# Kernel tuning notes

Hardware: AMD Instinct MI355X
Metric: run time of the kernel (lower is better)

## Reference

```python
import jax, jax.numpy as jnp
import numpy as np

B = 256      # batch
G = 16       # groups
GS = 588     # hard-coded group_size
HID = 1024   # hidden_dim (forced = hidden_dim3)
FEAT = 2048  # hidden_dim4 = per-group output feature dim


def setup_inputs() -> dict:
    key = jax.random.key(0)
    ks = jax.random.split(key, 16)
    def w(k, shape, fan_in):
        return jax.random.normal(k, shape, jnp.float32) / np.float32(np.sqrt(fan_in))
    inp = {
        "q": jax.random.normal(ks[0], (B, G * GS), jnp.float32),
        "k": jax.random.normal(ks[1], (B, G * GS), jnp.float32),
        # stacked per-group q-branch SVF weights: fc1 [G,GS,HID], fc4 [G,HID,FEAT]
        "Wq1": w(ks[2], (G, GS, HID), GS),
        "bq1": jnp.zeros((G, HID), jnp.float32),
        "Wq4": w(ks[3], (G, HID, FEAT), HID),
        "bq4": jnp.zeros((G, FEAT), jnp.float32),
        # stacked per-group k-branch SVF weights
        "Wk1": w(ks[4], (G, GS, HID), GS),
        "bk1": jnp.zeros((G, HID), jnp.float32),
        "Wk4": w(ks[5], (G, HID, FEAT), HID),
        "bk4": jnp.zeros((G, FEAT), jnp.float32),
        # shared global SVF: fc1 [G*FEAT, HID], fc4 [HID, FEAT]
        "Wg1": w(ks[6], (G * FEAT, HID), G * FEAT),
        "bg1": jnp.zeros((HID,), jnp.float32),
        "Wg4": w(ks[7], (HID, FEAT), HID),
        "bg4": jnp.zeros((FEAT,), jnp.float32),
    }
    return inp


def _grouped_svf(x, W1, b1, W4, b4):
    # x: [B, G*GS] -> per-group contiguous slices, batched grouped GEMMs
    xg = x.reshape(B, G, GS)
    h = jax.nn.silu(jnp.einsum('bgd,gdh->bgh', xg, W1) + b1)   # [B,G,HID]
    f = jax.nn.silu(jnp.einsum('bgh,gho->bgo', h, W4) + b4)    # [B,G,FEAT]
    # torch.stack(dim=2).view(B,-1): feature-major interleave [B, FEAT, G] -> flat
    return jnp.transpose(f, (0, 2, 1)).reshape(B, FEAT * G)


def _global_svf(x, Wg1, bg1, Wg4, bg4):
    h = jax.nn.silu(x @ Wg1 + bg1)      # [B, HID]
    return jax.nn.silu(h @ Wg4 + bg4)   # [B, FEAT]


def reference(q, k, Wq1, bq1, Wq4, bq4, Wk1, bk1, Wk4, bk4, Wg1, bg1, Wg4, bg4):
    qf = _grouped_svf(q, Wq1, bq1, Wq4, bq4)
    kf = _grouped_svf(k, Wk1, bk1, Wk4, bk4)
    q_out = _global_svf(qf, Wg1, bg1, Wg4, bg4)
    k_out = _global_svf(kf, Wg1, bg1, Wg4, bg4)
    scores = jnp.sum(q_out * k_out, axis=-1)   # [B]
    # faithful to original: softmax over the batch dimension
    return jax.nn.softmax(scores, axis=-1)
```

## Files before the change

### kernel.cpp

```cpp
#include <hip/hip_runtime.h>


#define CB 256
#define CG 16
#define CGS 588
#define CHID 1024
#define CFEAT 2048

typedef __attribute__((ext_vector_type(8))) short bf16x8;
typedef __attribute__((ext_vector_type(4))) float f32x4;

__device__ __forceinline__ int lds_addr(int row, int kcol) {
  return row * 64 + ((((kcol >> 3) ^ ((row >> 1) & 3)) << 4) | ((kcol & 7) << 1));
}

__device__ __forceinline__ void split4(const float4& v, uint2& hi, uint2& lo) {
  unsigned u0 = __float_as_uint(v.x), u1 = __float_as_uint(v.y);
  unsigned u2 = __float_as_uint(v.z), u3 = __float_as_uint(v.w);
  unsigned h0 = u0 & 0xffff0000u, h1 = u1 & 0xffff0000u;
  unsigned h2 = u2 & 0xffff0000u, h3 = u3 & 0xffff0000u;
  hi.x = (h0 >> 16) | h1;
  hi.y = (h2 >> 16) | h3;
  float r0 = v.x - __uint_as_float(h0), r1 = v.y - __uint_as_float(h1);
  float r2 = v.z - __uint_as_float(h2), r3 = v.w - __uint_as_float(h3);
  lo.x = (__float_as_uint(r0) >> 16) | (__float_as_uint(r1) & 0xffff0000u);
  lo.y = (__float_as_uint(r2) >> 16) | (__float_as_uint(r3) & 0xffff0000u);
}

__device__ __forceinline__ float silu_f(float x) {
  return x / (1.f + __expf(-x));
}

template <int GROUPED, int PERMUTE, int EPILOGUE>
__global__ __launch_bounds__(256, 2) void gemm_k(
    const float* __restrict__ A0, const float* __restrict__ A1,
    const float* __restrict__ B0, const float* __restrict__ B1,
    const float* __restrict__ bias0, const float* __restrict__ bias1,
    float* __restrict__ C, int K, int lda, int ldb, int ldc, int a_goff,
    long a_broff, long b_gstride, int bias_gstride, long c_broff, int c_goff,
    long c_sstride, int nksteps) {
  __shared__ __align__(16) char sm[32768];
  constexpr int A_HI = 0, A_LO = 8192, B_HI = 16384, B_LO = 24576;
  const int tid = threadIdx.x;
  const int m0 = blockIdx.x * 128, n0 = blockIdx.y * 128;

  const float* Ap;
  const float* Bp;
  const float* bp = nullptr;
  float* Cb;
  int acol = 0;
  int kbase = 0;
  if (GROUPED) {
    int z = blockIdx.z;
    int br = z >> 4, g = z & 15;
    Ap = (br ? A1 : A0) + (long)br * a_broff;
    Bp = (br ? B1 : B0) + (long)g * b_gstride;
    if (EPILOGUE) bp = (br ? bias1 : bias0) + (long)g * bias_gstride;
    Cb = C + (long)br * c_broff + (long)g * c_goff;
    acol = g * a_goff;
  } else {
    Ap = A0;
    Bp = B0;
    bp = bias0;
    Cb = C + (long)blockIdx.z * c_sstride;
    kbase = (int)blockIdx.z * nksteps * 32;
  }

  float4 ga[4];
  float gb[4][4];

  auto tload = [&](int k0) {
    const int r = tid >> 3, c4 = (tid & 7) << 2;
    const int gk = k0 + c4;
    #pragma unroll
    for (int i = 0; i < 4; ++i) {
      if (gk < K)
        ga[i] = *reinterpret_cast<const float4*>(Ap + (long)(m0 + i * 32 + r) * lda + acol + gk);
      else
        ga[i] = make_float4(0.f, 0.f, 0.f, 0.f);
    }
    const int n = tid & 127, kq0 = (tid >> 7) << 2;
    #pragma unroll
    for (int i = 0; i < 4; ++i) {
      #pragma unroll
      for (int j = 0; j < 4; ++j) {
        int kk = k0 + i * 8 + kq0 + j;
        float v = 0.f;
        if (kk < K) {
          long brow = PERMUTE ? (long)(((kk & 2047) << 4) | (kk >> 11)) : (long)kk;
          v = Bp[brow * ldb + n0 + n];
        }
        gb[i][j] = v;
      }
    }
  };

  auto tstore = [&]() {
    const int r = tid >> 3, c4 = (tid & 7) << 2;
    #pragma unroll
    for (int i = 0; i < 4; ++i) {
      uint2 h, l;
      split4(ga[i], h, l);
      int ad = lds_addr(i * 32 + r, c4);
      *reinterpret_cast<uint2*>(sm + A_HI + ad) = h;
      *reinterpret_cast<uint2*>(sm + A_LO + ad) = l;
    }
    const int n = tid & 127, kq0 = (tid >> 7) << 2;
    #pragma unroll
    for (int i = 0; i < 4; ++i) {
      float4 v = make_float4(gb[i][0], gb[i][1], gb[i][2], gb[i][3]);
      uint2 h, l;
      split4(v, h, l);
      int ad = lds_addr(n, i * 8 + kq0);
      *reinterpret_cast<uint2*>(sm + B_HI + ad) = h;
      *reinterpret_cast<uint2*>(sm + B_LO + ad) = l;
    }
  };

  f32x4 acc[4][4];
  #pragma unroll
  for (int a = 0; a < 4; ++a)
    #pragma unroll
    for (int b = 0; b < 4; ++b) acc[a][b] = (f32x4){0.f, 0.f, 0.f, 0.f};

  const int lane = tid & 63, w = tid >> 6;
  const int wr = w >> 1, wc = w & 1;
  const int fr = lane & 15, kb = lane >> 4;

  tload(kbase);
  for (int s = 0; s < nksteps; ++s) {
    tstore();
    __syncthreads();
    if (s + 1 < nksteps) tload(kbase + (s + 1) * 32);

    bf16x8 ah[4], al[4], bh[4], bl[4];
    #pragma unroll
    for (int f = 0; f < 4; ++f) {
      int row = wr * 64 + f * 16 + fr;
      int ad = row * 64 + ((kb ^ ((row >> 1) & 3)) << 4);
      ah[f] = *reinterpret_cast<const bf16x8*>(sm + A_HI + ad);
      al[f] = *reinterpret_cast<const bf16x8*>(sm + A_LO + ad);
      int rob = wc * 64 + f * 16 + fr;
      int bd = rob * 64 + ((kb ^ ((rob >> 1) & 3)) << 4);
      bh[f] = *reinterpret_cast<const bf16x8*>(sm + B_HI + bd);
      bl[f] = *reinterpret_cast<const bf16x8*>(sm + B_LO + bd);
    }
    #pragma unroll
    for (int im = 0; im < 4; ++im) {
      #pragma unroll
      for (int jn = 0; jn < 4; ++jn) {
        acc[im][jn] = __builtin_amdgcn_mfma_f32_16x16x32_bf16(ah[im], bh[jn], acc[im][jn], 0, 0, 0);
        acc[im][jn] = __builtin_amdgcn_mfma_f32_16x16x32_bf16(ah[im], bl[jn], acc[im][jn], 0, 0, 0);
        acc[im][jn] = __builtin_amdgcn_mfma_f32_16x16x32_bf16(al[im], bh[jn], acc[im][jn], 0, 0, 0);
      }
    }
    __syncthreads();
  }

  #pragma unroll
  for (int jn = 0; jn < 4; ++jn) {
    int col = n0 + wc * 64 + jn * 16 + fr;
    float bv = EPILOGUE ? bp[col] : 0.f;
    #pragma unroll
    for (int im = 0; im < 4; ++im) {
      int row0 = m0 + wr * 64 + im * 16 + kb * 4;
      #pragma unroll
      for (int j = 0; j < 4; ++j) {
        float x = acc[im][jn][j];
        if (EPILOGUE)
          Cb[(long)(row0 + j) * ldc + col] = silu_f(x + bv);
        else
          Cb[(long)(row0 + j) * ldc + col] = x;
      }
    }
  }
}

__global__ __launch_bounds__(256) void reduce_silu_k(
    const float* __restrict__ part, const float* __restrict__ bias,
    float* __restrict__ out, long MN, int N, int S) {
  long idx = ((long)blockIdx.x * blockDim.x + threadIdx.x) * 4;
  long stride = (long)gridDim.x * blockDim.x * 4;
  for (; idx < MN; idx += stride) {
    float4 a = make_float4(0.f, 0.f, 0.f, 0.f);
    for (int s = 0; s < S; ++s) {
      float4 p = *reinterpret_cast<const float4*>(&part[(long)s * MN + idx]);
      a.x += p.x; a.y += p.y; a.z += p.z; a.w += p.w;
    }
    int col = (int)(idx & (N - 1));
    float4 b = *reinterpret_cast<const float4*>(&bias[col]);
    float4 o;
    o.x = silu_f(a.x + b.x);
    o.y = silu_f(a.y + b.y);
    o.z = silu_f(a.z + b.z);
    o.w = silu_f(a.w + b.w);
    *reinterpret_cast<float4*>(&out[idx]) = o;
  }
}

__global__ __launch_bounds__(256) void scores_k(const float* __restrict__ out2,
                                                float* __restrict__ scores) {
  int b = blockIdx.x;
  const float* qo = out2 + (long)b * CFEAT;
  const float* ko = out2 + (long)(b + CB) * CFEAT;
  float s = 0.f;
  for (int i = threadIdx.x * 4; i < CFEAT; i += 1024) {
    float4 a = *reinterpret_cast<const float4*>(&qo[i]);
    float4 c = *reinterpret_cast<const float4*>(&ko[i]);
    s += a.x * c.x + a.y * c.y + a.z * c.z + a.w * c.w;
  }
  #pragma unroll
  for (int o = 32; o; o >>= 1) s += __shfl_down(s, o, 64);
  __shared__ float red[4];
  if ((threadIdx.x & 63) == 0) red[threadIdx.x >> 6] = s;
  __syncthreads();
  if (threadIdx.x == 0) scores[b] = red[0] + red[1] + red[2] + red[3];
}

__global__ __launch_bounds__(256) void softmax_k(const float* __restrict__ scores,
                                                 float* __restrict__ out) {
  int t = threadIdx.x;
  float v = scores[t];
  float m = v;
  #pragma unroll
  for (int o = 32; o; o >>= 1) m = fmaxf(m, __shfl_xor(m, o, 64));
  __shared__ float redm[4];
  if ((t & 63) == 0) redm[t >> 6] = m;
  __syncthreads();
  m = fmaxf(fmaxf(redm[0], redm[1]), fmaxf(redm[2], redm[3]));
  float e = __expf(v - m);
  float s = e;
  #pragma unroll
  for (int o = 32; o; o >>= 1) s += __shfl_xor(s, o, 64);
  __shared__ float reds[4];
  if ((t & 63) == 0) reds[t >> 6] = s;
  __syncthreads();
  s = reds[0] + reds[1] + reds[2] + reds[3];
  out[t] = e / s;
}

extern "C" void kernel_launch(void* const* d_in, const int* in_sizes, int n_in,
                              void* d_out, int out_size, void* d_ws,
                              size_t ws_size, hipStream_t stream) {
  const float* q   = (const float*)d_in[0];
  const float* kx  = (const float*)d_in[1];
  const float* Wq1 = (const float*)d_in[2];
  const float* bq1 = (const float*)d_in[3];
  const float* Wq4 = (const float*)d_in[4];
  const float* bq4 = (const float*)d_in[5];
  const float* Wk1 = (const float*)d_in[6];
  const float* bk1 = (const float*)d_in[7];
  const float* Wk4 = (const float*)d_in[8];
  const float* bk4 = (const float*)d_in[9];
  const float* Wg1 = (const float*)d_in[10];
  const float* bg1 = (const float*)d_in[11];
  const float* Wg4 = (const float*)d_in[12];
  const float* bg4 = (const float*)d_in[13];
  float* out = (float*)d_out;
  char* ws = (char*)d_ws;

  float* hqk   = (float*)(ws);
  float* fqk   = (float*)(ws + 33554432);
  float* part3 = (float*)(ws);
  float* h2    = (float*)(ws + 16777216);
  float* scors = (float*)(ws + 18874368);
  float* part4 = (float*)(ws + 33554432);
  float* out2  = (float*)(ws + 50331648);

  dim3 blk(256);

  gemm_k<1, 0, 1><<<dim3(2, 8, 32), blk, 0, stream>>>(
      q, kx, Wq1, Wk1, bq1, bk1, hqk,  CGS,  CG * CGS,
       CHID,  CG * CHID,  CGS,  0L,
       (long)CGS * CHID,  CHID,
       (long)CB * CG * CHID,  CHID, 0L,  19);

  gemm_k<1, 0, 1><<<dim3(2, 16, 32), blk, 0, stream>>>(
      hqk, hqk, Wq4, Wk4, bq4, bk4, fqk,  CHID,  CG * CHID,
       CFEAT,  CG * CFEAT,  CHID,
       (long)CB * CG * CHID,  (long)CHID * CFEAT,
       CFEAT,  (long)CB * CG * CFEAT,  CFEAT, 0L,
       32);

  gemm_k<0, 1, 0><<<dim3(4, 8, 8), blk, 0, stream>>>(
      fqk, fqk, Wg1, Wg1, bg1, bg1, part3,  CG * CFEAT,  CG * CFEAT,
       CHID,  CHID, 0, 0L, 0L, 0, 0L, 0,
       (long)512 * CHID,  128);
  reduce_silu_k<<<512, blk, 0, stream>>>(part3, bg1, h2, (long)512 * CHID, CHID, 8);

  gemm_k<0, 0, 0><<<dim3(4, 16, 4), blk, 0, stream>>>(
      h2, h2, Wg4, Wg4, bg4, bg4, part4,  CHID,  CHID,
       CFEAT,  CFEAT, 0, 0L, 0L, 0, 0L, 0,
       (long)512 * CFEAT,  8);
  reduce_silu_k<<<1024, blk, 0, stream>>>(part4, bg4, out2, (long)512 * CFEAT, CFEAT, 4);

  scores_k<<<256, blk, 0, stream>>>(out2, scors);
  softmax_k<<<1, blk, 0, stream>>>(scors, out);
}
```

Baseline: 753.9 us.

## Store intermediates as pre-split bf16 hi/lo planes and double split-K

Producer epilogues and the reduce kernel now write activations as separate bf16 high and low planes instead of fp32. Consumer GEMMs load these planes directly into LDS, which skips the per-tile split work and moves the same number of bytes per element. The split-K factor for both global GEMMs is also doubled, giving more blocks but more partial-sum traffic for the reduce kernels. Epilogue stores are scalar 2-byte writes to two planes, which may coalesce poorly.

New measurement: 1.043 ms. 1.38x slower.

```diff
diff --git a/kernel.cpp b/kernel.cpp
--- a/kernel.cpp
+++ b/kernel.cpp
@@ -31,12 +31,12 @@
   return x / (1.f + __expf(-x));
 }
 
-template <int GROUPED, int PERMUTE, int EPILOGUE>
+template <int GROUPED, int PERMUTE, int ASPLIT, int EPI>
 __global__ __launch_bounds__(256, 2) void gemm_k(
-    const float* __restrict__ A0, const float* __restrict__ A1,
+    const void* A0v, const void* A1v, long a_plane,
     const float* __restrict__ B0, const float* __restrict__ B1,
     const float* __restrict__ bias0, const float* __restrict__ bias1,
-    float* __restrict__ C, int K, int lda, int ldb, int ldc, int a_goff,
+    void* Cv, long c_plane, int K, int lda, int ldb, int ldc, int a_goff,
     long a_broff, long b_gstride, int bias_gstride, long c_broff, int c_goff,
     long c_sstride, int nksteps) {
   __shared__ __align__(16) char sm[32768];
@@ -44,40 +44,58 @@
   const int tid = threadIdx.x;
   const int m0 = blockIdx.x * 128, n0 = blockIdx.y * 128;
 
-  const float* Ap;
   const float* Bp;
   const float* bp = nullptr;
-  float* Cb;
+  const float* Af = nullptr;
+  const short* Ah = nullptr;
+  float* Cf = nullptr;
+  short* Chi = nullptr;
   int acol = 0;
   int kbase = 0;
   if (GROUPED) {
     int z = blockIdx.z;
     int br = z >> 4, g = z & 15;
-    Ap = (br ? A1 : A0) + (long)br * a_broff;
+    if (ASPLIT) Ah = (const short*)(br ? A1v : A0v) + (long)br * a_broff;
+    else        Af = (const float*)(br ? A1v : A0v) + (long)br * a_broff;
     Bp = (br ? B1 : B0) + (long)g * b_gstride;
-    if (EPILOGUE) bp = (br ? bias1 : bias0) + (long)g * bias_gstride;
-    Cb = C + (long)br * c_broff + (long)g * c_goff;
+    if (EPI) bp = (br ? bias1 : bias0) + (long)g * bias_gstride;
+    long coff = (long)br * c_broff + (long)g * c_goff;
+    if (EPI == 2) Chi = (short*)Cv + coff;
+    else          Cf = (float*)Cv + coff;
     acol = g * a_goff;
   } else {
-    Ap = A0;
+    if (ASPLIT) Ah = (const short*)A0v;
+    else        Af = (const float*)A0v;
     Bp = B0;
     bp = bias0;
-    Cb = C + (long)blockIdx.z * c_sstride;
+    if (EPI == 2) Chi = (short*)Cv;
+    else          Cf = (float*)Cv + (long)blockIdx.z * c_sstride;
     kbase = (int)blockIdx.z * nksteps * 32;
   }
 
   float4 ga[4];
+  uint4 gah[2], gal[2];
   float gb[4][4];
 
   auto tload = [&](int k0) {
-    const int r = tid >> 3, c4 = (tid & 7) << 2;
-    const int gk = k0 + c4;
-    #pragma unroll
-    for (int i = 0; i < 4; ++i) {
-      if (gk < K)
-        ga[i] = *reinterpret_cast<const float4*>(Ap + (long)(m0 + i * 32 + r) * lda + acol + gk);
-      else
-        ga[i] = make_float4(0.f, 0.f, 0.f, 0.f);
+    if (ASPLIT) {
+      #pragma unroll
+      for (int i = 0; i < 2; ++i) {
+        int u = tid + 256 * i, row = u >> 2, kq = u & 3;
+        long eo = (long)(m0 + row) * lda + acol + k0 + kq * 8;
+        gah[i] = *reinterpret_cast<const uint4*>(Ah + eo);
+        gal[i] = *reinterpret_cast<const uint4*>(Ah + a_plane + eo);
+      }
+    } else {
+      const int r = tid >> 3, c4 = (tid & 7) << 2;
+      const int gk = k0 + c4;
+      #pragma unroll
+      for (int i = 0; i < 4; ++i) {
+        if (gk < K)
+          ga[i] = *reinterpret_cast<const float4*>(Af + (long)(m0 + i * 32 + r) * lda + acol + gk);
+        else
+          ga[i] = make_float4(0.f, 0.f, 0.f, 0.f);
+      }
     }
     const int n = tid & 127, kq0 = (tid >> 7) << 2;
     #pragma unroll
@@ -96,14 +114,24 @@
   };
 
   auto tstore = [&]() {
-    const int r = tid >> 3, c4 = (tid & 7) << 2;
-    #pragma unroll
-    for (int i = 0; i < 4; ++i) {
-      uint2 h, l;
-      split4(ga[i], h, l);
-      int ad = lds_addr(i * 32 + r, c4);
-      *reinterpret_cast<uint2*>(sm + A_HI + ad) = h;
-      *reinterpret_cast<uint2*>(sm + A_LO + ad) = l;
+    if (ASPLIT) {
+      #pragma unroll
+      for (int i = 0; i < 2; ++i) {
+        int u = tid + 256 * i, row = u >> 2, kq = u & 3;
+        int ad = row * 64 + ((kq ^ ((row >> 1) & 3)) << 4);
+        *reinterpret_cast<uint4*>(sm + A_HI + ad) = gah[i];
+        *reinterpret_cast<uint4*>(sm + A_LO + ad) = gal[i];
+      }
+    } else {
+      const int r = tid >> 3, c4 = (tid & 7) << 2;
+      #pragma unroll
+      for (int i = 0; i < 4; ++i) {
+        uint2 h, l;
+        split4(ga[i], h, l);
+        int ad = lds_addr(i * 32 + r, c4);
+        *reinterpret_cast<uint2*>(sm + A_HI + ad) = h;
+        *reinterpret_cast<uint2*>(sm + A_LO + ad) = l;
+      }
     }
     const int n = tid & 127, kq0 = (tid >> 7) << 2;
     #pragma unroll
@@ -160,25 +188,35 @@
   #pragma unroll
   for (int jn = 0; jn < 4; ++jn) {
     int col = n0 + wc * 64 + jn * 16 + fr;
-    float bv = EPILOGUE ? bp[col] : 0.f;
+    float bv = EPI ? bp[col] : 0.f;
     #pragma unroll
     for (int im = 0; im < 4; ++im) {
       int row0 = m0 + wr * 64 + im * 16 + kb * 4;
       #pragma unroll
       for (int j = 0; j < 4; ++j) {
         float x = acc[im][jn][j];
-        if (EPILOGUE)
-          Cb[(long)(row0 + j) * ldc + col] = silu_f(x + bv);
-        else
-          Cb[(long)(row0 + j) * ldc + col] = x;
-      }
-    }
-  }
-}
-
+        long off = (long)(row0 + j) * ldc + col;
+        if (EPI == 2) {
+          float y = silu_f(x + bv);
+          unsigned u = __float_as_uint(y);
+          unsigned hu = u & 0xffff0000u;
+          float r = y - __uint_as_float(hu);
+          Chi[off] = (short)(hu >> 16);
+          Chi[c_plane + off] = (short)(__float_as_uint(r) >> 16);
+        } else if (EPI == 1) {
+          Cf[off] = silu_f(x + bv);
+        } else {
+          Cf[off] = x;
+        }
+      }
+    }
+  }
+}
+
+template <int SPLIT>
 __global__ __launch_bounds__(256) void reduce_silu_k(
     const float* __restrict__ part, const float* __restrict__ bias,
-    float* __restrict__ out, long MN, int N, int S) {
+    void* outv, long plane, long MN, int N, int S) {
   long idx = ((long)blockIdx.x * blockDim.x + threadIdx.x) * 4;
   long stride = (long)gridDim.x * blockDim.x * 4;
   for (; idx < MN; idx += stride) {
@@ -189,12 +227,29 @@
     }
     int col = (int)(idx & (N - 1));
     float4 b = *reinterpret_cast<const float4*>(&bias[col]);
-    float4 o;
-    o.x = silu_f(a.x + b.x);
-    o.y = silu_f(a.y + b.y);
-    o.z = silu_f(a.z + b.z);
-    o.w = silu_f(a.w + b.w);
-    *reinterpret_cast<float4*>(&out[idx]) = o;
+    float o[4];
+    o[0] = silu_f(a.x + b.x);
+    o[1] = silu_f(a.y + b.y);
+    o[2] = silu_f(a.z + b.z);
+    o[3] = silu_f(a.w + b.w);
+    if (SPLIT) {
+      unsigned u0 = __float_as_uint(o[0]) & 0xffff0000u;
+      unsigned u1 = __float_as_uint(o[1]) & 0xffff0000u;
+      unsigned u2 = __float_as_uint(o[2]) & 0xffff0000u;
+      unsigned u3 = __float_as_uint(o[3]) & 0xffff0000u;
+      uint2 hv, lv;
+      hv.x = (u0 >> 16) | u1;
+      hv.y = (u2 >> 16) | u3;
+      lv.x = (__float_as_uint(o[0] - __uint_as_float(u0)) >> 16) |
+             (__float_as_uint(o[1] - __uint_as_float(u1)) & 0xffff0000u);
+      lv.y = (__float_as_uint(o[2] - __uint_as_float(u2)) >> 16) |
+             (__float_as_uint(o[3] - __uint_as_float(u3)) & 0xffff0000u);
+      *reinterpret_cast<uint2*>((short*)outv + idx) = hv;
+      *reinterpret_cast<uint2*>((short*)outv + plane + idx) = lv;
+    } else {
+      float4 ov = make_float4(o[0], o[1], o[2], o[3]);
+      *reinterpret_cast<float4*>((float*)outv + idx) = ov;
+    }
   }
 }
 
@@ -259,40 +314,46 @@
   float* out = (float*)d_out;
   char* ws = (char*)d_ws;
 
-  float* hqk   = (float*)(ws);
-  float* fqk   = (float*)(ws + 33554432);
-  float* part3 = (float*)(ws);
-  float* h2    = (float*)(ws + 16777216);
-  float* scors = (float*)(ws + 18874368);
-  float* part4 = (float*)(ws + 33554432);
-  float* out2  = (float*)(ws + 50331648);
+  short* hqk_hi = (short*)ws;
+  const long hqk_plane = 8388608;
+  short* fqk_hi = (short*)(ws + 33554432);
+  const long fqk_plane = 16777216;
+  float* part3 = (float*)ws;
+  short* h2_hi = (short*)(ws + 33554432);
+  const long h2_plane = 524288;
+  float* part4 = (float*)(ws + 35651584);
+  float* out2  = (float*)(ws + 69206016);
+  float* scors = (float*)(ws + 73400320);
 
   dim3 blk(256);
 
-  gemm_k<1, 0, 1><<<dim3(2, 8, 32), blk, 0, stream>>>(
-      q, kx, Wq1, Wk1, bq1, bk1, hqk,  CGS,  CG * CGS,
-       CHID,  CG * CHID,  CGS,  0L,
-       (long)CGS * CHID,  CHID,
-       (long)CB * CG * CHID,  CHID, 0L,  19);
-
-  gemm_k<1, 0, 1><<<dim3(2, 16, 32), blk, 0, stream>>>(
-      hqk, hqk, Wq4, Wk4, bq4, bk4, fqk,  CHID,  CG * CHID,
-       CFEAT,  CG * CFEAT,  CHID,
-       (long)CB * CG * CHID,  (long)CHID * CFEAT,
-       CFEAT,  (long)CB * CG * CFEAT,  CFEAT, 0L,
-       32);
-
-  gemm_k<0, 1, 0><<<dim3(4, 8, 8), blk, 0, stream>>>(
-      fqk, fqk, Wg1, Wg1, bg1, bg1, part3,  CG * CFEAT,  CG * CFEAT,
-       CHID,  CHID, 0, 0L, 0L, 0, 0L, 0,
-       (long)512 * CHID,  128);
-  reduce_silu_k<<<512, blk, 0, stream>>>(part3, bg1, h2, (long)512 * CHID, CHID, 8);
-
-  gemm_k<0, 0, 0><<<dim3(4, 16, 4), blk, 0, stream>>>(
-      h2, h2, Wg4, Wg4, bg4, bg4, part4,  CHID,  CHID,
-       CFEAT,  CFEAT, 0, 0L, 0L, 0, 0L, 0,
-       (long)512 * CFEAT,  8);
-  reduce_silu_k<<<1024, blk, 0, stream>>>(part4, bg4, out2, (long)512 * CFEAT, CFEAT, 4);
+  gemm_k<1, 0, 0, 2><<<dim3(2, 8, 32), blk, 0, stream>>>(
+      q, kx, 0L, Wq1, Wk1, bq1, bk1, hqk_hi, hqk_plane,
+       CGS,  CG * CGS,  CHID,  CG * CHID,
+       CGS,  0L,  (long)CGS * CHID,
+       CHID,  (long)CB * CG * CHID,  CHID, 0L,
+       19);
+
+  gemm_k<1, 0, 1, 2><<<dim3(2, 16, 32), blk, 0, stream>>>(
+      hqk_hi, hqk_hi, hqk_plane, Wq4, Wk4, bq4, bk4, fqk_hi, fqk_plane,
+       CHID,  CG * CHID,  CFEAT,  CG * CFEAT,
+       CHID,  (long)CB * CG * CHID,
+       (long)CHID * CFEAT,  CFEAT,
+       (long)CB * CG * CFEAT,  CFEAT, 0L,  32);
+
+  gemm_k<0, 1, 1, 0><<<dim3(4, 8, 16), blk, 0, stream>>>(
+      fqk_hi, fqk_hi, fqk_plane, Wg1, Wg1, bg1, bg1, part3, 0L,
+       CG * CFEAT,  CG * CFEAT,  CHID,  CHID, 0, 0L,
+      0L, 0, 0L, 0,  (long)512 * CHID,  64);
+  reduce_silu_k<1><<<512, blk, 0, stream>>>(part3, bg1, h2_hi, h2_plane,
+                                            (long)512 * CHID, CHID, 16);
+
+  gemm_k<0, 0, 1, 0><<<dim3(4, 16, 8), blk, 0, stream>>>(
+      h2_hi, h2_hi, h2_plane, Wg4, Wg4, bg4, bg4, part4, 0L,
+       CHID,  CHID,  CFEAT,  CFEAT, 0, 0L, 0L, 0, 0L,
+      0,  (long)512 * CFEAT,  4);
+  reduce_silu_k<0><<<1024, blk, 0, stream>>>(part4, bg4, out2, 0L,
+                                             (long)512 * CFEAT, CFEAT, 8);
 
   scores_k<<<256, blk, 0, stream>>>(out2, scors);
   softmax_k<<<1, blk, 0, stream>>>(scors, out);
```

## Store intermediate activations as pre-split bf16 hi/lo planes and template GEMM shapes

Applied to the files above, without the earlier changes.

Intermediate activations (padded q/k, hidden, features, global hidden) are now written once as bf16 hi/lo planes by the producing kernel, staged through LDS for coalesced stores. The GEMM A-operand then loads pre-split bf16 data directly instead of loading fp32 and splitting per tile, which cuts A-side bandwidth and conversion ALU work. GEMM dimensions become template constants, and split-K for the two global GEMMs is doubled. The costs are an extra conversion kernel for q/k, more epilogue LDS traffic, and more partial-sum traffic in the reductions.

After: 1.012 ms. 34.2% more time.

```diff
diff --git a/kernel.cpp b/kernel.cpp
--- a/kernel.cpp
+++ b/kernel.cpp
@@ -9,10 +9,6 @@
 
 typedef __attribute__((ext_vector_type(8))) short bf16x8;
 typedef __attribute__((ext_vector_type(4))) float f32x4;
-
-__device__ __forceinline__ int lds_addr(int row, int kcol) {
-  return row * 64 + ((((kcol >> 3) ^ ((row >> 1) & 3)) << 4) | ((kcol & 7) << 1));
-}
 
 __device__ __forceinline__ void split4(const float4& v, uint2& hi, uint2& lo) {
   unsigned u0 = __float_as_uint(v.x), u1 = __float_as_uint(v.y);
@@ -27,174 +23,226 @@
   lo.y = (__float_as_uint(r2) >> 16) | (__float_as_uint(r3) & 0xffff0000u);
 }
 
-__device__ __forceinline__ float silu_f(float x) {
-  return x / (1.f + __expf(-x));
-}
-
-template <int GROUPED, int PERMUTE, int EPILOGUE>
+__device__ __forceinline__ float silu_f(float x) { return x / (1.f + __expf(-x)); }
+
+__global__ __launch_bounds__(256) void conv_qk_k(const float* __restrict__ q,
+                                                 const float* __restrict__ kx,
+                                                 short* __restrict__ out) {
+  const int idx = blockIdx.x * 256 + threadIdx.x;
+  if (idx >= 2 * CB * CG * 152) return;
+  const int kp4 = (idx % 152) * 4;
+  int rest = idx / 152;
+  const int g = rest & 15;
+  rest >>= 4;
+  const int b = rest & 255;
+  const int br = rest >> 8;
+  float4 v = make_float4(0.f, 0.f, 0.f, 0.f);
+  if (kp4 < CGS)
+    v = *reinterpret_cast<const float4*>((br ? kx : q) + (long)b * (CG * CGS) + g * CGS + kp4);
+  uint2 h, l;
+  split4(v, h, l);
+  const long off = ((long)(br * CB + b) * CG + g) * 608 + kp4;
+  *reinterpret_cast<uint2*>(out + off) = h;
+  *reinterpret_cast<uint2*>(out + 4980736 + off) = l;
+}
+
+template <int KTOT, int LDA, int LDB, int LDC, int NK, int GROUPED, int PERMUTE,
+          int EPI, int BMAX>
 __global__ __launch_bounds__(256, 2) void gemm_k(
-    const float* __restrict__ A0, const float* __restrict__ A1,
-    const float* __restrict__ B0, const float* __restrict__ B1,
+    const short* __restrict__ A, long a_plane, long a_broff, int a_goff,
+    const float* __restrict__ B0, const float* __restrict__ B1, long b_gstride,
     const float* __restrict__ bias0, const float* __restrict__ bias1,
-    float* __restrict__ C, int K, int lda, int ldb, int ldc, int a_goff,
-    long a_broff, long b_gstride, int bias_gstride, long c_broff, int c_goff,
-    long c_sstride, int nksteps) {
-  __shared__ __align__(16) char sm[32768];
+    int bias_g, void* Cv, long c_plane, long c_broff, int c_goff,
+    long c_sstride) {
+  __shared__ __align__(16) char sm[34816];
   constexpr int A_HI = 0, A_LO = 8192, B_HI = 16384, B_LO = 24576;
   const int tid = threadIdx.x;
   const int m0 = blockIdx.x * 128, n0 = blockIdx.y * 128;
-
-  const float* Ap;
+  const int z = blockIdx.z;
+
+  const short* Ab;
   const float* Bp;
-  const float* bp = nullptr;
-  float* Cb;
-  int acol = 0;
+  const float* bp;
+  long cbase;
   int kbase = 0;
   if (GROUPED) {
-    int z = blockIdx.z;
-    int br = z >> 4, g = z & 15;
-    Ap = (br ? A1 : A0) + (long)br * a_broff;
+    const int br = z >> 4, g = z & 15;
+    Ab = A + (long)br * a_broff + (long)g * a_goff;
     Bp = (br ? B1 : B0) + (long)g * b_gstride;
-    if (EPILOGUE) bp = (br ? bias1 : bias0) + (long)g * bias_gstride;
-    Cb = C + (long)br * c_broff + (long)g * c_goff;
-    acol = g * a_goff;
+    bp = (br ? bias1 : bias0) + (long)g * bias_g;
+    cbase = (long)br * c_broff + (long)g * c_goff;
   } else {
-    Ap = A0;
+    Ab = A;
     Bp = B0;
     bp = bias0;
-    Cb = C + (long)blockIdx.z * c_sstride;
-    kbase = (int)blockIdx.z * nksteps * 32;
-  }
-
-  float4 ga[4];
+    cbase = (long)z * c_sstride;
+    kbase = z * NK * 32;
+  }
+
+  const int arow = tid >> 2, akq = tid & 3;
+  const int bn = tid & 127, bk0 = (tid >> 7) << 2;
+
+  uint4 gah[2], gal[2];
   float gb[4][4];
 
-  auto tload = [&](int k0) {
-    const int r = tid >> 3, c4 = (tid & 7) << 2;
-    const int gk = k0 + c4;
-    #pragma unroll
-    for (int i = 0; i < 4; ++i) {
-      if (gk < K)
-        ga[i] = *reinterpret_cast<const float4*>(Ap + (long)(m0 + i * 32 + r) * lda + acol + gk);
-      else
-        ga[i] = make_float4(0.f, 0.f, 0.f, 0.f);
-    }
-    const int n = tid & 127, kq0 = (tid >> 7) << 2;
-    #pragma unroll
-    for (int i = 0; i < 4; ++i) {
-      #pragma unroll
-      for (int j = 0; j < 4; ++j) {
-        int kk = k0 + i * 8 + kq0 + j;
-        float v = 0.f;
-        if (kk < K) {
-          long brow = PERMUTE ? (long)(((kk & 2047) << 4) | (kk >> 11)) : (long)kk;
-          v = Bp[brow * ldb + n0 + n];
-        }
-        gb[i][j] = v;
-      }
-    }
-  };
-
-  auto tstore = [&]() {
-    const int r = tid >> 3, c4 = (tid & 7) << 2;
-    #pragma unroll
-    for (int i = 0; i < 4; ++i) {
-      uint2 h, l;
-      split4(ga[i], h, l);
-      int ad = lds_addr(i * 32 + r, c4);
-      *reinterpret_cast<uint2*>(sm + A_HI + ad) = h;
-      *reinterpret_cast<uint2*>(sm + A_LO + ad) = l;
-    }
-    const int n = tid & 127, kq0 = (tid >> 7) << 2;
+#define LOAD_TILE(K0)                                                          \
+  {                                                                            \
+    _Pragma("unroll") for (int i = 0; i < 2; ++i) {                            \
+      const long eo = (long)(m0 + arow + 64 * i) * LDA + (K0) + akq * 8;       \
+      gah[i] = *reinterpret_cast<const uint4*>(Ab + eo);                       \
+      gal[i] = *reinterpret_cast<const uint4*>(Ab + a_plane + eo);             \
+    }                                                                          \
+    _Pragma("unroll") for (int i = 0; i < 4; ++i) {                            \
+      _Pragma("unroll") for (int j = 0; j < 4; ++j) {                          \
+        const int kk = (K0) + i * 8 + bk0 + j;                                 \
+        float v = 0.f;                                                         \
+        if (BMAX == KTOT || kk < BMAX) {                                       \
+          const long brow =                                                    \
+              PERMUTE ? (long)(((kk & 2047) << 4) | (kk >> 11)) : (long)kk;    \
+          v = Bp[brow * LDB + n0 + bn];                                        \
+        }                                                                      \
+        gb[i][j] = v;                                                          \
+      }                                                                        \
+    }                                                                          \
+  }
+
+  f32x4 acc[4][4];
+  #pragma unroll
+  for (int a = 0; a < 4; ++a)
+    #pragma unroll
+    for (int b = 0; b < 4; ++b) acc[a][b] = (f32x4){0.f, 0.f, 0.f, 0.f};
+
+  const int lane = tid & 63, w = tid >> 6;
+  const int wr = w >> 1, wc = w & 1;
+  const int fr = lane & 15, kb = lane >> 4;
+
+  LOAD_TILE(kbase)
+  for (int s = 0; s < NK; ++s) {
+    #pragma unroll
+    for (int i = 0; i < 2; ++i) {
+      const int row = arow + 64 * i;
+      const int ad = row * 64 + ((akq ^ ((row >> 1) & 3)) << 4);
+      *reinterpret_cast<uint4*>(sm + A_HI + ad) = gah[i];
+      *reinterpret_cast<uint4*>(sm + A_LO + ad) = gal[i];
+    }
     #pragma unroll
     for (int i = 0; i < 4; ++i) {
       float4 v = make_float4(gb[i][0], gb[i][1], gb[i][2], gb[i][3]);
       uint2 h, l;
       split4(v, h, l);
-      int ad = lds_addr(n, i * 8 + kq0);
+      const int kcol = i * 8 + bk0;
+      const int ad = bn * 64 + (((kcol >> 3) ^ ((bn >> 1) & 3)) << 4) +
+                     ((kcol & 7) << 1);
       *reinterpret_cast<uint2*>(sm + B_HI + ad) = h;
       *reinterpret_cast<uint2*>(sm + B_LO + ad) = l;
     }
-  };
-
-  f32x4 acc[4][4];
-  #pragma unroll
-  for (int a = 0; a < 4; ++a)
-    #pragma unroll
-    for (int b = 0; b < 4; ++b) acc[a][b] = (f32x4){0.f, 0.f, 0.f, 0.f};
-
-  const int lane = tid & 63, w = tid >> 6;
-  const int wr = w >> 1, wc = w & 1;
-  const int fr = lane & 15, kb = lane >> 4;
-
-  tload(kbase);
-  for (int s = 0; s < nksteps; ++s) {
-    tstore();
     __syncthreads();
-    if (s + 1 < nksteps) tload(kbase + (s + 1) * 32);
-
-    bf16x8 ah[4], al[4], bh[4], bl[4];
+    if (s + 1 < NK) LOAD_TILE(kbase + (s + 1) * 32)
+
+    bf16x8 bh[4], bl[4];
     #pragma unroll
     for (int f = 0; f < 4; ++f) {
-      int row = wr * 64 + f * 16 + fr;
-      int ad = row * 64 + ((kb ^ ((row >> 1) & 3)) << 4);
-      ah[f] = *reinterpret_cast<const bf16x8*>(sm + A_HI + ad);
-      al[f] = *reinterpret_cast<const bf16x8*>(sm + A_LO + ad);
-      int rob = wc * 64 + f * 16 + fr;
-      int bd = rob * 64 + ((kb ^ ((rob >> 1) & 3)) << 4);
+      const int rob = wc * 64 + f * 16 + fr;
+      const int bd = rob * 64 + ((kb ^ ((rob >> 1) & 3)) << 4);
       bh[f] = *reinterpret_cast<const bf16x8*>(sm + B_HI + bd);
       bl[f] = *reinterpret_cast<const bf16x8*>(sm + B_LO + bd);
     }
     #pragma unroll
     for (int im = 0; im < 4; ++im) {
+      const int row = wr * 64 + im * 16 + fr;
+      const int ad = row * 64 + ((kb ^ ((row >> 1) & 3)) << 4);
+      bf16x8 ah = *reinterpret_cast<const bf16x8*>(sm + A_HI + ad);
+      bf16x8 al = *reinterpret_cast<const bf16x8*>(sm + A_LO + ad);
       #pragma unroll
       for (int jn = 0; jn < 4; ++jn) {
-        acc[im][jn] = __builtin_amdgcn_mfma_f32_16x16x32_bf16(ah[im], bh[jn], acc[im][jn], 0, 0, 0);
-        acc[im][jn] = __builtin_amdgcn_mfma_f32_16x16x32_bf16(ah[im], bl[jn], acc[im][jn], 0, 0, 0);
-        acc[im][jn] = __builtin_amdgcn_mfma_f32_16x16x32_bf16(al[im], bh[jn], acc[im][jn], 0, 0, 0);
+        acc[im][jn] = __builtin_amdgcn_mfma_f32_16x16x32_bf16(ah, bh[jn], acc[im][jn], 0, 0, 0);
+        acc[im][jn] = __builtin_amdgcn_mfma_f32_16x16x32_bf16(ah, bl[jn], acc[im][jn], 0, 0, 0);
+        acc[im][jn] = __builtin_amdgcn_mfma_f32_16x16x32_bf16(al, bh[jn], acc[im][jn], 0, 0, 0);
       }
     }
     __syncthreads();
   }
-
-  #pragma unroll
-  for (int jn = 0; jn < 4; ++jn) {
-    int col = n0 + wc * 64 + jn * 16 + fr;
-    float bv = EPILOGUE ? bp[col] : 0.f;
-    #pragma unroll
-    for (int im = 0; im < 4; ++im) {
-      int row0 = m0 + wr * 64 + im * 16 + kb * 4;
-      #pragma unroll
-      for (int j = 0; j < 4; ++j) {
-        float x = acc[im][jn][j];
-        if (EPILOGUE)
-          Cb[(long)(row0 + j) * ldc + col] = silu_f(x + bv);
-        else
-          Cb[(long)(row0 + j) * ldc + col] = x;
+#undef LOAD_TILE
+
+  if (EPI == 2) {
+    #pragma unroll
+    for (int jn = 0; jn < 4; ++jn) {
+      const float bv = bp[n0 + wc * 64 + jn * 16 + fr];
+      #pragma unroll
+      for (int im = 0; im < 4; ++im)
+        #pragma unroll
+        for (int j = 0; j < 4; ++j)
+          acc[im][jn][j] = silu_f(acc[im][jn][j] + bv);
+    }
+    short* smS = (short*)sm;
+    short* Cs = (short*)Cv;
+    #pragma unroll
+    for (int p = 0; p < 2; ++p) {
+      #pragma unroll
+      for (int im = 0; im < 4; ++im)
+        #pragma unroll
+        for (int jn = 0; jn < 4; ++jn)
+          #pragma unroll
+          for (int j = 0; j < 4; ++j) {
+            const int row = wr * 64 + im * 16 + kb * 4 + j;
+            const int col = wc * 64 + jn * 16 + fr;
+            const float y = acc[im][jn][j];
+            const unsigned hu = __float_as_uint(y) & 0xffff0000u;
+            const unsigned val =
+                p == 0 ? (hu >> 16)
+                       : (__float_as_uint(y - __uint_as_float(hu)) >> 16);
+            smS[row * 136 + col] = (short)val;
+          }
+      __syncthreads();
+      #pragma unroll
+      for (int e = 0; e < 8; ++e) {
+        const int S = (tid + 256 * e) * 8;
+        const int row = S >> 7, col = S & 127;
+        uint4 v = *reinterpret_cast<const uint4*>(smS + row * 136 + col);
+        *reinterpret_cast<uint4*>(Cs + p * c_plane + cbase +
+                                  (long)(m0 + row) * LDC + n0 + col) = v;
       }
-    }
-  }
-}
-
+      if (p == 0) __syncthreads();
+    }
+  } else {
+    float* Cf = (float*)Cv + cbase;
+    #pragma unroll
+    for (int jn = 0; jn < 4; ++jn) {
+      const int col = n0 + wc * 64 + jn * 16 + fr;
+      #pragma unroll
+      for (int im = 0; im < 4; ++im) {
+        const int row0 = m0 + wr * 64 + im * 16 + kb * 4;
+        #pragma unroll
+        for (int j = 0; j < 4; ++j)
+          Cf[(long)(row0 + j) * LDC + col] = acc[im][jn][j];
+      }
+    }
+  }
+}
+
+template <int SPLIT>
 __global__ __launch_bounds__(256) void reduce_silu_k(
     const float* __restrict__ part, const float* __restrict__ bias,
-    float* __restrict__ out, long MN, int N, int S) {
+    void* outv, long plane, long MN, int N, int S) {
   long idx = ((long)blockIdx.x * blockDim.x + threadIdx.x) * 4;
-  long stride = (long)gridDim.x * blockDim.x * 4;
-  for (; idx < MN; idx += stride) {
-    float4 a = make_float4(0.f, 0.f, 0.f, 0.f);
-    for (int s = 0; s < S; ++s) {
-      float4 p = *reinterpret_cast<const float4*>(&part[(long)s * MN + idx]);
-      a.x += p.x; a.y += p.y; a.z += p.z; a.w += p.w;
-    }
-    int col = (int)(idx & (N - 1));
-    float4 b = *reinterpret_cast<const float4*>(&bias[col]);
-    float4 o;
-    o.x = silu_f(a.x + b.x);
-    o.y = silu_f(a.y + b.y);
-    o.z = silu_f(a.z + b.z);
-    o.w = silu_f(a.w + b.w);
-    *reinterpret_cast<float4*>(&out[idx]) = o;
+  if (idx >= MN) return;
+  float4 a = make_float4(0.f, 0.f, 0.f, 0.f);
+  for (int s = 0; s < S; ++s) {
+    float4 p = *reinterpret_cast<const float4*>(&part[(long)s * MN + idx]);
+    a.x += p.x; a.y += p.y; a.z += p.z; a.w += p.w;
+  }
+  const int col = (int)(idx & (N - 1));
+  float4 b = *reinterpret_cast<const float4*>(&bias[col]);
+  float o0 = silu_f(a.x + b.x), o1 = silu_f(a.y + b.y);
+  float o2 = silu_f(a.z + b.z), o3 = silu_f(a.w + b.w);
+  if (SPLIT) {
+    float4 ov = make_float4(o0, o1, o2, o3);
+    uint2 hv, lv;
+    split4(ov, hv, lv);
+    *reinterpret_cast<uint2*>((short*)outv + idx) = hv;
+    *reinterpret_cast<uint2*>((short*)outv + plane + idx) = lv;
+  } else {
+    *reinterpret_cast<float4*>((float*)outv + idx) = make_float4(o0, o1, o2, o3);
   }
 }
 
@@ -259,40 +307,42 @@
   float* out = (float*)d_out;
   char* ws = (char*)d_ws;
 
-  float* hqk   = (float*)(ws);
-  float* fqk   = (float*)(ws + 33554432);
-  float* part3 = (float*)(ws);
-  float* h2    = (float*)(ws + 16777216);
-  float* scors = (float*)(ws + 18874368);
-  float* part4 = (float*)(ws + 33554432);
-  float* out2  = (float*)(ws + 50331648);
+  short* qkpad = (short*)ws;
+  short* fqk   = (short*)ws;
+  short* hqk   = (short*)(ws + 67108864);
+  float* part3 = (float*)(ws + 67108864);
+  short* h2    = (short*)ws;
+  float* part4 = (float*)(ws + 67108864);
+  float* out2  = (float*)(ws + 4194304);
+  float* scors = (float*)(ws + 8388608);
 
   dim3 blk(256);
 
-  gemm_k<1, 0, 1><<<dim3(2, 8, 32), blk, 0, stream>>>(
-      q, kx, Wq1, Wk1, bq1, bk1, hqk,  CGS,  CG * CGS,
-       CHID,  CG * CHID,  CGS,  0L,
-       (long)CGS * CHID,  CHID,
-       (long)CB * CG * CHID,  CHID, 0L,  19);
-
-  gemm_k<1, 0, 1><<<dim3(2, 16, 32), blk, 0, stream>>>(
-      hqk, hqk, Wq4, Wk4, bq4, bk4, fqk,  CHID,  CG * CHID,
-       CFEAT,  CG * CFEAT,  CHID,
-       (long)CB * CG * CHID,  (long)CHID * CFEAT,
-       CFEAT,  (long)CB * CG * CFEAT,  CFEAT, 0L,
-       32);
-
-  gemm_k<0, 1, 0><<<dim3(4, 8, 8), blk, 0, stream>>>(
-      fqk, fqk, Wg1, Wg1, bg1, bg1, part3,  CG * CFEAT,  CG * CFEAT,
-       CHID,  CHID, 0, 0L, 0L, 0, 0L, 0,
-       (long)512 * CHID,  128);
-  reduce_silu_k<<<512, blk, 0, stream>>>(part3, bg1, h2, (long)512 * CHID, CHID, 8);
-
-  gemm_k<0, 0, 0><<<dim3(4, 16, 4), blk, 0, stream>>>(
-      h2, h2, Wg4, Wg4, bg4, bg4, part4,  CHID,  CHID,
-       CFEAT,  CFEAT, 0, 0L, 0L, 0, 0L, 0,
-       (long)512 * CFEAT,  8);
-  reduce_silu_k<<<1024, blk, 0, stream>>>(part4, bg4, out2, (long)512 * CFEAT, CFEAT, 4);
+  conv_qk_k<<<4864, blk, 0, stream>>>(q, kx, qkpad);
+
+  gemm_k<608, 9728, CHID, CG * CHID, 19, 1, 0, 2, 588>
+      <<<dim3(2, 8, 32), blk, 0, stream>>>(
+          qkpad, 4980736L, 2490368L, 608, Wq1, Wk1, (long)CGS * CHID, bq1, bk1,
+          CHID, hqk, 8388608L, 4194304L, CHID, 0L);
+
+  gemm_k<CHID, CG * CHID, CFEAT, CG * CFEAT, 32, 1, 0, 2, CHID>
+      <<<dim3(2, 16, 32), blk, 0, stream>>>(
+          hqk, 8388608L, 4194304L, CHID, Wq4, Wk4, (long)CHID * CFEAT, bq4, bk4,
+          CFEAT, fqk, 16777216L, 8388608L, CFEAT, 0L);
+
+  gemm_k<CG * CFEAT, CG * CFEAT, CHID, CHID, 64, 0, 1, 0, CG * CFEAT>
+      <<<dim3(4, 8, 16), blk, 0, stream>>>(
+          fqk, 16777216L, 0L, 0, Wg1, Wg1, 0L, bg1, bg1, 0, part3, 0L, 0L, 0,
+          (long)512 * CHID);
+  reduce_silu_k<1><<<512, blk, 0, stream>>>(part3, bg1, h2, 524288L,
+                                            (long)512 * CHID, CHID, 16);
+
+  gemm_k<CHID, CHID, CFEAT, CFEAT, 4, 0, 0, 0, CHID>
+      <<<dim3(4, 16, 8), blk, 0, stream>>>(
+          h2, 524288L, 0L, 0, Wg4, Wg4, 0L, bg4, bg4, 0, part4, 0L, 0L, 0,
+          (long)512 * CFEAT);
+  reduce_silu_k<0><<<1024, blk, 0, stream>>>(part4, bg4, out2, 0L,
+                                             (long)512 * CFEAT, CFEAT, 8);
 
   scores_k<<<256, blk, 0, stream>>>(out2, scors);
   softmax_k<<<1, blk, 0, stream>>>(scors, out);
```
